# Optimization experiments

Measured on AMD Instinct MI355X. Metric: run time of the kernel, lower is better.

Reference implementation:

```python
import jax, jax.numpy as jnp
import numpy as np

NT, NRV, NR = 100000, 200000, 300000  # tile / road_vertex / road node counts
E = 400000                             # edges per edge type
B, H, P, A = 64, 128, 64, 512          # graphs, hidden, player_state_dim, action_dim


def _gat(h_src, h_dst, src, dst, W, a_s, a_d, b, n_dst):
    # PyG GATConv, heads=1, shared lin for src/dst, no self loops (bipartite)
    hs = h_src @ W                      # [Ns, H]
    hd = h_dst @ W                      # [Nd, H]
    e = jax.nn.leaky_relu((hs @ a_s)[src] + (hd @ a_d)[dst], 0.2)  # [E]
    m = jax.ops.segment_max(e, dst, num_segments=n_dst)
    w = jnp.exp(e - m[dst])
    denom = jax.ops.segment_sum(w, dst, num_segments=n_dst)
    alpha = w / jnp.maximum(denom[dst], 1e-16)                      # segment softmax
    out = jax.ops.segment_sum(alpha[:, None] * hs[src], dst, num_segments=n_dst)
    return out + b


def _mean_pool(x, batch, nb):
    s = jax.ops.segment_sum(x, batch, num_segments=nb)
    c = jax.ops.segment_sum(jnp.ones((x.shape[0],), x.dtype), batch, num_segments=nb)
    return s / jnp.maximum(c, 1.0)[:, None]


def setup_inputs():
    ks = iter(jax.random.split(jax.random.key(0), 64))
    f32 = jnp.float32

    def lin(i, o):
        return (jax.random.normal(next(ks), (i, o), f32) / np.float32(np.sqrt(i)))

    d = {}
    d['x_tile'] = jax.random.normal(next(ks), (NT, 8), f32)
    d['x_rv'] = jax.random.normal(next(ks), (NRV, 13), f32)
    d['x_road'] = jax.random.normal(next(ks), (NR, 4), f32)
    d['x_player'] = jax.random.normal(next(ks), (B, P), f32)
    # node encoders
    d['enc_t_W'] = lin(8, H);  d['enc_t_b'] = jnp.zeros((H,), f32)
    d['enc_rv_W'] = lin(13, H); d['enc_rv_b'] = jnp.zeros((H,), f32)
    d['enc_r_W'] = lin(4, H);  d['enc_r_b'] = jnp.zeros((H,), f32)
    # six GAT convs
    for name in ['rv2t', 't2rv', 'r2rv', 'rv2r', 't2r', 'r2t']:
        d[name + '_W'] = lin(H, H)
        d[name + '_as'] = jax.random.normal(next(ks), (H,), f32) * 0.1
        d[name + '_ad'] = jax.random.normal(next(ks), (H,), f32) * 0.1
        d[name + '_b'] = jnp.zeros((H,), f32)
    # player MLP + output head (input: 3H pooled + H player)
    d['fc1_W'] = lin(P, H); d['fc1_b'] = jnp.zeros((H,), f32)
    d['fc2_W'] = lin(H, H); d['fc2_b'] = jnp.zeros((H,), f32)
    d['out_W'] = lin(4 * H, A); d['out_b'] = jnp.zeros((A,), f32)
    # edges (src bounded by source-type count, dst by dest-type count)
    ri = lambda n, hi: jax.random.randint(n, (E,), 0, hi, jnp.int32)
    d['e_rv2t_src'] = ri(next(ks), NRV); d['e_rv2t_dst'] = ri(next(ks), NT)
    d['e_t2rv_src'] = ri(next(ks), NT);  d['e_t2rv_dst'] = ri(next(ks), NRV)
    d['e_r2rv_src'] = ri(next(ks), NR);  d['e_r2rv_dst'] = ri(next(ks), NRV)
    d['e_rv2r_src'] = ri(next(ks), NRV); d['e_rv2r_dst'] = ri(next(ks), NR)
    d['e_t2r_src'] = ri(next(ks), NT);   d['e_t2r_dst'] = ri(next(ks), NR)
    d['e_r2t_src'] = ri(next(ks), NR);   d['e_r2t_dst'] = ri(next(ks), NT)
    # batch assignment per node type
    d['batch_tile'] = jnp.sort(jax.random.randint(next(ks), (NT,), 0, B, jnp.int32))
    d['batch_rv'] = jnp.sort(jax.random.randint(next(ks), (NRV,), 0, B, jnp.int32))
    d['batch_road'] = jnp.sort(jax.random.randint(next(ks), (NR,), 0, B, jnp.int32))
    return d


def reference(x_tile, x_rv, x_road, x_player,
              enc_t_W, enc_t_b, enc_rv_W, enc_rv_b, enc_r_W, enc_r_b,
              rv2t_W, rv2t_as, rv2t_ad, rv2t_b,
              t2rv_W, t2rv_as, t2rv_ad, t2rv_b,
              r2rv_W, r2rv_as, r2rv_ad, r2rv_b,
              rv2r_W, rv2r_as, rv2r_ad, rv2r_b,
              t2r_W, t2r_as, t2r_ad, t2r_b,
              r2t_W, r2t_as, r2t_ad, r2t_b,
              fc1_W, fc1_b, fc2_W, fc2_b, out_W, out_b,
              e_rv2t_src, e_rv2t_dst, e_t2rv_src, e_t2rv_dst,
              e_r2rv_src, e_r2rv_dst, e_rv2r_src, e_rv2r_dst,
              e_t2r_src, e_t2r_dst, e_r2t_src, e_r2t_dst,
              batch_tile, batch_rv, batch_road):
    # node encoders
    h_t = x_tile @ enc_t_W + enc_t_b
    h_rv = x_rv @ enc_rv_W + enc_rv_b
    h_r = x_road @ enc_r_W + enc_r_b
    # hetero GAT, aggr='sum' over edge types per destination node type
    o_t = (_gat(h_rv, h_t, e_rv2t_src, e_rv2t_dst, rv2t_W, rv2t_as, rv2t_ad, rv2t_b, NT)
           + _gat(h_r, h_t, e_r2t_src, e_r2t_dst, r2t_W, r2t_as, r2t_ad, r2t_b, NT))
    o_rv = (_gat(h_t, h_rv, e_t2rv_src, e_t2rv_dst, t2rv_W, t2rv_as, t2rv_ad, t2rv_b, NRV)
            + _gat(h_r, h_rv, e_r2rv_src, e_r2rv_dst, r2rv_W, r2rv_as, r2rv_ad, r2rv_b, NRV))
    o_r = (_gat(h_rv, h_r, e_rv2r_src, e_rv2r_dst, rv2r_W, rv2r_as, rv2r_ad, rv2r_b, NR)
           + _gat(h_t, h_r, e_t2r_src, e_t2r_dst, t2r_W, t2r_as, t2r_ad, t2r_b, NR))
    # global mean pool per node type, concat -> [B, 3H]
    x_all = jnp.concatenate([_mean_pool(o_t, batch_tile, B),
                             _mean_pool(o_rv, batch_rv, B),
                             _mean_pool(o_r, batch_road, B)], axis=1)
    # player branch
    p = jax.nn.relu(x_player @ fc1_W + fc1_b)
    p = jax.nn.relu(p @ fc2_W + fc2_b)
    x = jnp.concatenate([x_all, p], axis=1)  # [B, 4H]
    return x @ out_W + out_b                 # [B, A]
```

## Files before the change

kernel.cpp:

```cpp
#include <hip/hip_runtime.h>


constexpr int kNT = 100000, kNRV = 200000, kNR = 300000, kE = 400000;
constexpr int kSLOT = 1088;
constexpr int kPSZ  = 6 * kSLOT;
constexpr int kNBE  = 342;
constexpr int kNTH  = kNBE * 256;
constexpr int kEPT  = 5;

constexpr long long OFF_C    = 0;
constexpr long long OFF_VS   = 13056;
constexpr long long OFF_VD   = 13176;
constexpr long long OFF_P    = 13296;
constexpr long long OFF_XCAT = 19824;
constexpr long long OFF_SRV  = 52592;
constexpr long long OFF_ST   = 3252592;
constexpr long long OFF_SR   = 4052592;
constexpr long long OFF_LDD  = 5252592;
constexpr long long OFF_P8   = 7652592;

__constant__ const int kDRB[6]   = {0, 100000, 300000, 500000, 800000, 1100000};
__constant__ const int kDLEN[6]  = {100000, 200000, 200000, 300000, 300000, 100000};
__constant__ const int kLSOFF[6] = {7, 4, 2, 8, 5, 3};
__constant__ const int kRSZ[6]   = {16, 8, 4, 16, 8, 4};

__device__ __forceinline__ int lowb(const int* a, int n, int v) {
  int lo = 0, hi = n;
  while (lo < hi) { int mid = (lo + hi) >> 1; if (a[mid] < v) lo = mid + 1; else hi = mid; }
  return lo;
}

static __device__ __forceinline__ unsigned p2h(float a, float b) {
  _Float16 ha = (_Float16)a, hb = (_Float16)b;
  unsigned short ua = __builtin_bit_cast(unsigned short, ha);
  unsigned short ub = __builtin_bit_cast(unsigned short, hb);
  return (unsigned)ua | ((unsigned)ub << 16);
}

static __device__ __forceinline__ float emb(float ld, int b) {
  return __uint_as_float((__float_as_uint(ld) & ~63u) | (unsigned)b);
}

__global__ __launch_bounds__(256) void precompute_kernel(
    const float* encW_t, const float* encb_t,
    const float* encW_rv, const float* encb_rv,
    const float* encW_r, const float* encb_r,
    const float* W0, const float* as0, const float* ad0,
    const float* W1, const float* as1, const float* ad1,
    const float* W2, const float* as2, const float* ad2,
    const float* W3, const float* as3, const float* ad3,
    const float* W4, const float* as4, const float* ad4,
    const float* W5, const float* as5, const float* ad5,
    float* Cws, float* vsw, float* vdw, float* P8)
{
  const float* encW[3] = {encW_t, encW_rv, encW_r};
  const float* encb[3] = {encb_t, encb_rv, encb_r};
  const int    Ks[3]   = {8, 13, 4};
  const float* Wv[6]  = {W0, W1, W2, W3, W4, W5};
  const float* asv[6] = {as0, as1, as2, as3, as4, as5};
  const float* adv[6] = {ad0, ad1, ad2, ad3, ad4, ad5};
  const int srcT[6] = {1, 0, 2, 1, 0, 2};
  const int dstT[6] = {0, 1, 1, 2, 2, 0};

  __shared__ float Cl[2176];
  __shared__ float wv[128];

  int et = blockIdx.x;
  int tid = threadIdx.x;
  int st = srcT[et], dt = dstT[et];
  const float* eW = encW[st];
  const float* eB = encb[st];
  int K = Ks[st];
  const float* W = Wv[et];
  const float* a_s = asv[et];
  const float* a_d = adv[et];
  float* Cslot = Cws + et * 2176;

  for (int c = 0; c < 8; ++c)
    for (int i = tid; i < kSLOT; i += 256)
      P8[c * kPSZ + et * kSLOT + i] = 0.f;

  for (int idx = tid; idx < (K + 1) * 128; idx += 256) {
    int r = idx >> 7, j = idx & 127;
    const float* row = (r < K) ? (eW + r * 128) : eB;
    float acc = 0.f;
    for (int m = 0; m < 128; ++m) acc += row[m] * W[m * 128 + j];
    int o = (r < K) ? (r * 128 + j) : (2048 + j);
    Cl[o] = acc;
    Cslot[o] = acc;
  }
  if (tid < 128) {
    float acc = 0.f;
    for (int j = 0; j < 128; ++j) acc += W[tid * 128 + j] * a_d[j];
    wv[tid] = acc;
  }
  __syncthreads();
  if (tid <= K) {
    const float* row = (tid < K) ? (Cl + tid * 128) : (Cl + 2048);
    float acc = 0.f;
    for (int j = 0; j < 128; ++j) acc += row[j] * a_s[j];
    vsw[et * 20 + (tid < K ? tid : 16)] = acc;
  }
  int KD = Ks[dt];
  if (tid >= 32 && tid <= 32 + KD) {
    int k = tid - 32;
    const float* row = (k < KD) ? (encW[dt] + k * 128) : encb[dt];
    float acc = 0.f;
    for (int m = 0; m < 128; ++m) acc += row[m] * wv[m];
    vdw[et * 20 + (k < KD ? k : 16)] = acc;
  }
}

__global__ __launch_bounds__(256) void prep_kernel(
    const float* __restrict__ x_t, const float* __restrict__ x_rv,
    const float* __restrict__ x_r,
    const int* __restrict__ bt, const int* __restrict__ brv,
    const int* __restrict__ br,
    const float* __restrict__ vsw, const float* __restrict__ vdw,
    uint4* __restrict__ SRVq, uint4* __restrict__ STq, uint4* __restrict__ SRq,
    float* __restrict__ LDDf)
{
  int n = blockIdx.x * 256 + threadIdx.x;
  if (n >= kNT + kNRV + kNR) return;
  if (n < kNT) {
    const float* xr = x_t + n * 8;
    int b = bt[n];
    const float* vsA = vsw + 1 * 20, *vsB = vsw + 4 * 20;
    const float* vdA = vdw + 0 * 20, *vdB = vdw + 5 * 20;
    float x[8]; float a0 = 0, a1 = 0, a2 = 0, a3 = 0;
#pragma unroll
    for (int k = 0; k < 8; ++k) {
      x[k] = xr[k];
      a0 += x[k] * vsA[k]; a1 += x[k] * vsB[k];
      a2 += x[k] * vdA[k]; a3 += x[k] * vdB[k];
    }
    float ls1 = a0 + vsA[16], ls4 = a1 + vsB[16];
    float ld0 = a2 + vdA[16], ld5 = a3 + vdB[16];
    STq[(long long)n * 2] =
        make_uint4(p2h(x[0], x[1]), p2h(x[2], x[3]), p2h(x[4], x[5]), p2h(x[6], x[7]));
    STq[(long long)n * 2 + 1] =
        make_uint4(__float_as_uint(ls1), __float_as_uint(ls4), 0, 0);
    LDDf[(long long)n * 2] = emb(ld0, b);
    LDDf[(long long)n * 2 + 1] = 0.f;
    LDDf[(long long)(1100000 + n) * 2] = emb(ld5, b);
    LDDf[(long long)(1100000 + n) * 2 + 1] = 0.f;
  } else if (n < kNT + kNRV) {
    int m = n - kNT;
    const float* xr = x_rv + m * 13;
    int b = brv[m];
    const float* vsA = vsw + 0 * 20, *vsB = vsw + 3 * 20;
    const float* vdA = vdw + 1 * 20, *vdB = vdw + 2 * 20;
    float x[13]; float a0 = 0, a1 = 0, a2 = 0, a3 = 0;
#pragma unroll
    for (int k = 0; k < 13; ++k) {
      x[k] = xr[k];
      a0 += x[k] * vsA[k]; a1 += x[k] * vsB[k];
      a2 += x[k] * vdA[k]; a3 += x[k] * vdB[k];
    }
    float ls0 = a0 + vsA[16], ls3 = a1 + vsB[16];
    float ld1 = a2 + vdA[16], ld2 = a3 + vdB[16];
    SRVq[(long long)m * 4] =
        make_uint4(p2h(x[0], x[1]), p2h(x[2], x[3]), p2h(x[4], x[5]), p2h(x[6], x[7]));
    SRVq[(long long)m * 4 + 1] =
        make_uint4(p2h(x[8], x[9]), p2h(x[10], x[11]), p2h(x[12], 0.f),
                   __float_as_uint(ls0));
    SRVq[(long long)m * 4 + 2] = make_uint4(__float_as_uint(ls3), 0, 0, 0);
    LDDf[(long long)(100000 + m) * 2] = emb(ld1, b);
    LDDf[(long long)(100000 + m) * 2 + 1] = 0.f;
    LDDf[(long long)(300000 + m) * 2] = emb(ld2, b);
    LDDf[(long long)(300000 + m) * 2 + 1] = 0.f;
  } else {
    int m = n - kNT - kNRV;
    const float* xr = x_r + m * 4;
    int b = br[m];
    const float* vsA = vsw + 2 * 20, *vsB = vsw + 5 * 20;
    const float* vdA = vdw + 3 * 20, *vdB = vdw + 4 * 20;
    float x[4]; float a0 = 0, a1 = 0, a2 = 0, a3 = 0;
#pragma unroll
    for (int k = 0; k < 4; ++k) {
      x[k] = xr[k];
      a0 += x[k] * vsA[k]; a1 += x[k] * vsB[k];
      a2 += x[k] * vdA[k]; a3 += x[k] * vdB[k];
    }
    float ls2 = a0 + vsA[16], ls5 = a1 + vsB[16];
    float ld3 = a2 + vdA[16], ld4 = a3 + vdB[16];
    SRq[m] = make_uint4(p2h(x[0], x[1]), p2h(x[2], x[3]),
                        __float_as_uint(ls2), __float_as_uint(ls5));
    LDDf[(long long)(500000 + m) * 2] = emb(ld3, b);
    LDDf[(long long)(500000 + m) * 2 + 1] = 0.f;
    LDDf[(long long)(800000 + m) * 2] = emb(ld4, b);
    LDDf[(long long)(800000 + m) * 2 + 1] = 0.f;
  }
}

__device__ __forceinline__ void pickSD(
    int et,
    const int* s0, const int* s1, const int* s2,
    const int* s3, const int* s4, const int* s5,
    const int* d0, const int* d1, const int* d2,
    const int* d3, const int* d4, const int* d5,
    const int*& sp, const int*& dp)
{
  switch (et) {
    case 0: sp = s0; dp = d0; break;
    case 1: sp = s1; dp = d1; break;
    case 2: sp = s2; dp = d2; break;
    case 3: sp = s3; dp = d3; break;
    case 4: sp = s4; dp = d4; break;
    default: sp = s5; dp = d5; break;
  }
}

__global__ __launch_bounds__(256, 8) void edgeA_kernel(
    const int* s0, const int* s1, const int* s2,
    const int* s3, const int* s4, const int* s5,
    const int* d0, const int* d1, const int* d2,
    const int* d3, const int* d4, const int* d5,
    const unsigned* __restrict__ SRVu, const unsigned* __restrict__ STu,
    const unsigned* __restrict__ SRu, float* __restrict__ LDDf)
{
  int et = blockIdx.x / kNBE;
  int bIdx = blockIdx.x - et * kNBE;
  const int* sp; const int* dp;
  pickSD(et, s0, s1, s2, s3, s4, s5, d0, d1, d2, d3, d4, d5, sp, dp);
  const unsigned* su = (et == 1 || et == 4) ? STu : ((et == 2 || et == 5) ? SRu : SRVu);
  const int rsz = kRSZ[et];
  const int lso = kLSOFF[et];
  const int drb = kDRB[et];
  int base = bIdx * 256 + (int)threadIdx.x;

  int s[kEPT], d[kEPT]; bool ok[kEPT];
#pragma unroll
  for (int j = 0; j < kEPT; ++j) {
    int e = base + j * kNTH;
    ok[j] = e < kE;
    int ee = ok[j] ? e : 0;
    s[j] = sp[ee]; d[j] = dp[ee];
  }
  float ls[kEPT];
#pragma unroll
  for (int j = 0; j < kEPT; ++j)
    ls[j] = __uint_as_float(su[(long long)s[j] * rsz + lso]);
  float ld[kEPT];
#pragma unroll
  for (int j = 0; j < kEPT; ++j)
    ld[j] = LDDf[(long long)(drb + d[j]) * 2];
#pragma unroll
  for (int j = 0; j < kEPT; ++j) {
    float t = ls[j] + ld[j];
    t = t > 0.f ? t : 0.2f * t;
    float w = __expf(t);
    if (ok[j]) unsafeAtomicAdd(&LDDf[(long long)(drb + d[j]) * 2 + 1], w);
  }
}

template <int TYPE, int RSEL>
__device__ __forceinline__ void ebflow(
    int bIdx,
    const int* __restrict__ sp, const int* __restrict__ dp,
    const uint4* __restrict__ srq, const float2* __restrict__ LDD2,
    int drb, int dlen, float* lp)
{
  constexpr int K = (TYPE == 0) ? 8 : ((TYPE == 1) ? 13 : 4);
  const int tid = threadIdx.x;
  const int lane = tid & 63;
  int base = bIdx * 256 + tid;

  int s[kEPT], d[kEPT]; bool ok[kEPT];
#pragma unroll
  for (int j = 0; j < kEPT; ++j) {
    int e = base + j * kNTH;
    ok[j] = e < kE;
    int ee = ok[j] ? e : 0;
    s[j] = sp[ee]; d[j] = dp[ee];
  }
  uint4 q0[kEPT], q1[kEPT];
  float lsx[kEPT];
#pragma unroll
  for (int j = 0; j < kEPT; ++j) {
    if (TYPE == 0) {
      q0[j] = srq[(long long)s[j] * 2];
      lsx[j] = __uint_as_float(
          ((const unsigned*)srq)[(long long)s[j] * 8 + (RSEL ? 5 : 4)]);
    } else if (TYPE == 1) {
      q0[j] = srq[(long long)s[j] * 4];
      q1[j] = srq[(long long)s[j] * 4 + 1];
      lsx[j] = RSEL
          ? __uint_as_float(((const unsigned*)srq)[(long long)s[j] * 16 + 8])
          : __uint_as_float(q1[j].w);
    } else {
      q0[j] = srq[s[j]];
      lsx[j] = __uint_as_float(RSEL ? q0[j].w : q0[j].z);
    }
  }
  float2 f2[kEPT];
#pragma unroll
  for (int j = 0; j < kEPT; ++j) f2[j] = LDD2[drb + d[j]];

#pragma unroll
  for (int j = 0; j < kEPT; ++j) {
    if (!ok[j]) continue;
    int b = (int)(__float_as_uint(f2[j].x) & 63u);
    float t = lsx[j] + f2[j].x;
    t = t > 0.f ? t : 0.2f * t;
    float w = __expf(t);
    float alpha = w / fmaxf(f2[j].y, 1e-16f);
    float xv[K];
    if (TYPE == 0) {
      const _Float16* h = (const _Float16*)&q0[j];
#pragma unroll
      for (int k = 0; k < 8; ++k) xv[k] = (float)h[k];
    } else if (TYPE == 1) {
      const _Float16* h = (const _Float16*)&q0[j];
#pragma unroll
      for (int k = 0; k < 8; ++k) xv[k] = (float)h[k];
      const _Float16* h2 = (const _Float16*)&q1[j];
#pragma unroll
      for (int k = 0; k < 5; ++k) xv[8 + k] = (float)h2[k];
    } else {
      const _Float16* h = (const _Float16*)&q0[j];
#pragma unroll
      for (int k = 0; k < 4; ++k) xv[k] = (float)h[k];
    }
#pragma unroll
    for (int k = 0; k < K; ++k) atomicAdd(lp + k * 64 + b, alpha * xv[k]);
  }

  for (int base2 = bIdx * 256 + (tid & ~63); base2 < dlen; base2 += kNTH) {
    int j2 = base2 + lane;
    bool a2 = j2 < dlen;
    float2 r2 = a2 ? LDD2[drb + j2] : make_float2(0.f, 0.f);
    int b2 = a2 ? (int)(__float_as_uint(r2.x) & 63u) : (64 + lane);
    int v = (a2 && r2.y > 0.f) ? 1 : 0;
#pragma unroll
    for (int d2 = 1; d2 < 64; d2 <<= 1) {
      int ob = __shfl_up(b2, d2);
      int ov = __shfl_up(v, d2);
      if (lane >= d2 && ob == b2) v += ov;
    }
    int bn = __shfl_down(b2, 1);
    if (((lane == 63) || (bn != b2)) && v > 0) atomicAdd(lp + 1024 + b2, (float)v);
  }
}

__global__ __launch_bounds__(256, 4) void edgeB_kernel(
    const int* s0, const int* s1, const int* s2,
    const int* s3, const int* s4, const int* s5,
    const int* d0, const int* d1, const int* d2,
    const int* d3, const int* d4, const int* d5,
    const uint4* SRVq, const uint4* STq, const uint4* SRq,
    const float2* __restrict__ LDD2, float* __restrict__ P8)
{
  __shared__ float lp[kSLOT];
  for (int j = threadIdx.x; j < kSLOT; j += 256) lp[j] = 0.f;
  __syncthreads();
  int et = blockIdx.x / kNBE;
  int bIdx = blockIdx.x - et * kNBE;
  constexpr int KK[6] = {13, 8, 4, 13, 8, 4};
  switch (et) {
    case 0: ebflow<1, 0>(bIdx, s0, d0, SRVq, LDD2, 0,       100000, lp); break;
    case 1: ebflow<0, 0>(bIdx, s1, d1, STq,  LDD2, 100000,  200000, lp); break;
    case 2: ebflow<2, 0>(bIdx, s2, d2, SRq,  LDD2, 300000,  200000, lp); break;
    case 3: ebflow<1, 1>(bIdx, s3, d3, SRVq, LDD2, 500000,  300000, lp); break;
    case 4: ebflow<0, 1>(bIdx, s4, d4, STq,  LDD2, 800000,  300000, lp); break;
    default: ebflow<2, 1>(bIdx, s5, d5, SRq, LDD2, 1100000, 100000, lp); break;
  }
  __syncthreads();
  int K = KK[et];
  float* slab = P8 + (long long)(blockIdx.x & 7) * kPSZ + (long long)et * kSLOT;
  for (int i = threadIdx.x; i < kSLOT; i += 256) {
    if (i >= K * 64 && i < 1024) continue;
    float v = lp[i];
    if (v != 0.f) unsafeAtomicAdd(&slab[i], v);
  }
}

__global__ __launch_bounds__(256) void reduceP8_kernel(
    const float* __restrict__ P8, float* __restrict__ P)
{
  int j = blockIdx.x * 256 + threadIdx.x;
  if (j >= kPSZ) return;
  float s = 0.f;
#pragma unroll
  for (int c = 0; c < 8; ++c) s += P8[c * kPSZ + j];
  P[j] = s;
}

__global__ __launch_bounds__(128) void finalize_kernel(
    const int* __restrict__ bt, const int* __restrict__ brv, const int* __restrict__ br,
    const float* __restrict__ xp,
    const float* __restrict__ fc1W, const float* __restrict__ fc1b,
    const float* __restrict__ fc2W, const float* __restrict__ fc2b,
    const float* __restrict__ b_rv2t, const float* __restrict__ b_r2t,
    const float* __restrict__ b_t2rv, const float* __restrict__ b_r2rv,
    const float* __restrict__ b_rv2r, const float* __restrict__ b_t2r,
    const float* __restrict__ Cws, const float* __restrict__ P,
    float* __restrict__ xcat)
{
  int b = blockIdx.x, tid = threadIdx.x;
  __shared__ float xps[64];
  __shared__ float p1s[128];
  __shared__ int cnts[3];
  if (tid < 64) xps[tid] = xp[b * 64 + tid];
  if (tid < 3) {
    const int* ba = (tid == 0) ? bt : (tid == 1 ? brv : br);
    int N = (tid == 0) ? kNT : (tid == 1 ? kNRV : kNR);
    cnts[tid] = lowb(ba, N, b + 1) - lowb(ba, N, b);
  }
  __syncthreads();
  float a = fc1b[tid];
  for (int k = 0; k < 64; ++k) a += xps[k] * fc1W[k * 128 + tid];
  p1s[tid] = fmaxf(a, 0.f);
  __syncthreads();
  float a2 = fc2b[tid];
  for (int k = 0; k < 128; ++k) a2 += p1s[k] * fc2W[k * 128 + tid];
  xcat[b * 512 + 384 + tid] = fmaxf(a2, 0.f);
  const int etA[3] = {0, 1, 3}, etB[3] = {5, 2, 4};
  const int KAv[3] = {13, 8, 13}, KBv[3] = {4, 4, 8};
  for (int t3 = 0; t3 < 3; ++t3) {
    int eA = etA[t3], eB = etB[t3];
    const float* CA = Cws + eA * 2176;
    const float* CB = Cws + eB * 2176;
    const float* pA = P + eA * kSLOT;
    const float* pB = P + eB * kSLOT;
    float cA = pA[1024 + b];
    float cB = pB[1024 + b];
    float v = cA * CA[2048 + tid] + cB * CB[2048 + tid];
    for (int k = 0; k < KAv[t3]; ++k) v += pA[k * 64 + b] * CA[k * 128 + tid];
    for (int k = 0; k < KBv[t3]; ++k) v += pB[k * 64 + b] * CB[k * 128 + tid];
    float cnt = (float)max(cnts[t3], 1);
    const float* bb1 = (t3 == 0) ? b_rv2t : (t3 == 1 ? b_t2rv : b_rv2r);
    const float* bb2 = (t3 == 0) ? b_r2t  : (t3 == 1 ? b_r2rv : b_t2r);
    xcat[b * 512 + t3 * 128 + tid] = v / cnt + bb1[tid] + bb2[tid];
  }
}

__global__ __launch_bounds__(256) void out_kernel(
    const float* __restrict__ xcat, const float* __restrict__ outW,
    const float* __restrict__ outb, float* __restrict__ out)
{
  int g = blockIdx.x * 256 + threadIdx.x;
  int r = g >> 9, c = g & 511;
  const float* xr = xcat + r * 512;
  float acc = outb[c];
  for (int k = 0; k < 512; ++k) acc += xr[k] * outW[k * 512 + c];
  out[g] = acc;
}

extern "C" void kernel_launch(void* const* d_in, const int* in_sizes, int n_in,
                              void* d_out, int out_size, void* d_ws, size_t ws_size,
                              hipStream_t stream) {
  const float* x_tile   = (const float*)d_in[0];
  const float* x_rv     = (const float*)d_in[1];
  const float* x_road   = (const float*)d_in[2];
  const float* x_player = (const float*)d_in[3];
  const float* enc_t_W  = (const float*)d_in[4];
  const float* enc_t_b  = (const float*)d_in[5];
  const float* enc_rv_W = (const float*)d_in[6];
  const float* enc_rv_b = (const float*)d_in[7];
  const float* enc_r_W  = (const float*)d_in[8];
  const float* enc_r_b  = (const float*)d_in[9];
  const float* W[6]; const float* As[6]; const float* Ad[6]; const float* Bb[6];
  for (int et = 0; et < 6; ++et) {
    W[et]  = (const float*)d_in[10 + 4 * et];
    As[et] = (const float*)d_in[11 + 4 * et];
    Ad[et] = (const float*)d_in[12 + 4 * et];
    Bb[et] = (const float*)d_in[13 + 4 * et];
  }
  const float* fc1W = (const float*)d_in[34];
  const float* fc1b = (const float*)d_in[35];
  const float* fc2W = (const float*)d_in[36];
  const float* fc2b = (const float*)d_in[37];
  const float* outW = (const float*)d_in[38];
  const float* outb = (const float*)d_in[39];
  const int* esrc[6]; const int* edst[6];
  for (int et = 0; et < 6; ++et) {
    esrc[et] = (const int*)d_in[40 + 2 * et];
    edst[et] = (const int*)d_in[41 + 2 * et];
  }
  const int* batch_t  = (const int*)d_in[52];
  const int* batch_rv = (const int*)d_in[53];
  const int* batch_r  = (const int*)d_in[54];

  float* wsF = (float*)d_ws;
  float* Cws  = wsF + OFF_C;
  float* vsw  = wsF + OFF_VS;
  float* vdw  = wsF + OFF_VD;
  float* P    = wsF + OFF_P;
  float* xcat = wsF + OFF_XCAT;
  uint4* SRVq = (uint4*)(wsF + OFF_SRV);
  uint4* STq  = (uint4*)(wsF + OFF_ST);
  uint4* SRq  = (uint4*)(wsF + OFF_SR);
  float* LDDf = wsF + OFF_LDD;
  float2* LDD2 = (float2*)(wsF + OFF_LDD);
  float* P8   = wsF + OFF_P8;
  float* out  = (float*)d_out;

  precompute_kernel<<<6, 256, 0, stream>>>(
      enc_t_W, enc_t_b, enc_rv_W, enc_rv_b, enc_r_W, enc_r_b,
      W[0], As[0], Ad[0], W[1], As[1], Ad[1], W[2], As[2], Ad[2],
      W[3], As[3], Ad[3], W[4], As[4], Ad[4], W[5], As[5], Ad[5],
      Cws, vsw, vdw, P8);

  prep_kernel<<<(kNT + kNRV + kNR + 255) / 256, 256, 0, stream>>>(
      x_tile, x_rv, x_road, batch_t, batch_rv, batch_r, vsw, vdw,
      SRVq, STq, SRq, LDDf);

  edgeA_kernel<<<6 * kNBE, 256, 0, stream>>>(
      esrc[0], esrc[1], esrc[2], esrc[3], esrc[4], esrc[5],
      edst[0], edst[1], edst[2], edst[3], edst[4], edst[5],
      (const unsigned*)SRVq, (const unsigned*)STq, (const unsigned*)SRq, LDDf);

  edgeB_kernel<<<6 * kNBE, 256, 0, stream>>>(
      esrc[0], esrc[1], esrc[2], esrc[3], esrc[4], esrc[5],
      edst[0], edst[1], edst[2], edst[3], edst[4], edst[5],
      SRVq, STq, SRq, LDD2, P8);

  reduceP8_kernel<<<(kPSZ + 255) / 256, 256, 0, stream>>>(P8, P);

  finalize_kernel<<<64, 128, 0, stream>>>(
      batch_t, batch_rv, batch_r, x_player,
      fc1W, fc1b, fc2W, fc2b,
      Bb[0], Bb[5], Bb[1], Bb[2], Bb[3], Bb[4],
      Cws, P, xcat);

  out_kernel<<<128, 256, 0, stream>>>(xcat, outW, outb, out);

  (void)in_sizes; (void)n_in; (void)out_size; (void)ws_size;
}
```

Before: 527.0 us.

## Fuse P8 reduction, finalize and output GEMM into one tail kernel; compact source logits

The reduceP8, finalize and out kernels are merged into a single tail kernel with one block per graph. Each block recomputes the encoder-times-W projections in shared memory and sums the eight P8 partial copies itself, which cuts two launches and the xcat round trip. Precompute now only folds W with the attention vectors, and its P8 zeroing is spread across all six blocks. prep writes a compact float array of source logits, so edgeA gathers 4-byte values instead of reading them from strided packed rows. The cost is redundant per-block projection work (64 blocks doing the same 128x128 by K products) and low parallelism in the fused output GEMM.

```diff
diff --git a/kernel.cpp b/kernel.cpp
--- a/kernel.cpp
+++ b/kernel.cpp
@@ -8,21 +8,18 @@
 constexpr int kNTH  = kNBE * 256;
 constexpr int kEPT  = 5;
 
-constexpr long long OFF_C    = 0;
-constexpr long long OFF_VS   = 13056;
-constexpr long long OFF_VD   = 13176;
-constexpr long long OFF_P    = 13296;
-constexpr long long OFF_XCAT = 19824;
-constexpr long long OFF_SRV  = 52592;
-constexpr long long OFF_ST   = 3252592;
-constexpr long long OFF_SR   = 4052592;
-constexpr long long OFF_LDD  = 5252592;
-constexpr long long OFF_P8   = 7652592;
-
-__constant__ const int kDRB[6]   = {0, 100000, 300000, 500000, 800000, 1100000};
-__constant__ const int kDLEN[6]  = {100000, 200000, 200000, 300000, 300000, 100000};
-__constant__ const int kLSOFF[6] = {7, 4, 2, 8, 5, 3};
-__constant__ const int kRSZ[6]   = {16, 8, 4, 16, 8, 4};
+constexpr long long OFF_VS   = 0;
+constexpr long long OFF_VD   = 120;
+constexpr long long OFF_P8   = 256;
+constexpr long long OFF_LS6  = 52480;
+constexpr long long OFF_SRV  = 652480;
+constexpr long long OFF_ST   = 3852480;
+constexpr long long OFF_SR   = 4652480;
+constexpr long long OFF_LDD  = 5852480;
+
+__constant__ const int kDRB[6]  = {0, 100000, 300000, 500000, 800000, 1100000};
+__constant__ const int kDLEN[6] = {100000, 200000, 200000, 300000, 300000, 100000};
+__constant__ const int kLSB6[6] = {0, 400000, 0, 200000, 500000, 0};
 
 __device__ __forceinline__ int lowb(const int* a, int n, int v) {
   int lo = 0, hi = n;
@@ -51,7 +48,7 @@
     const float* W3, const float* as3, const float* ad3,
     const float* W4, const float* as4, const float* ad4,
     const float* W5, const float* as5, const float* ad5,
-    float* Cws, float* vsw, float* vdw, float* P8)
+    float* vsw, float* vdw, float* P8)
 {
   const float* encW[3] = {encW_t, encW_rv, encW_r};
   const float* encb[3] = {encb_t, encb_rv, encb_r};
@@ -62,43 +59,34 @@
   const int srcT[6] = {1, 0, 2, 1, 0, 2};
   const int dstT[6] = {0, 1, 1, 2, 2, 0};
 
-  __shared__ float Cl[2176];
-  __shared__ float wv[128];
+  __shared__ float ws[128], wd[128];
 
   int et = blockIdx.x;
   int tid = threadIdx.x;
   int st = srcT[et], dt = dstT[et];
-  const float* eW = encW[st];
-  const float* eB = encb[st];
-  int K = Ks[st];
   const float* W = Wv[et];
   const float* a_s = asv[et];
   const float* a_d = adv[et];
-  float* Cslot = Cws + et * 2176;
-
-  for (int c = 0; c < 8; ++c)
-    for (int i = tid; i < kSLOT; i += 256)
-      P8[c * kPSZ + et * kSLOT + i] = 0.f;
-
-  for (int idx = tid; idx < (K + 1) * 128; idx += 256) {
-    int r = idx >> 7, j = idx & 127;
-    const float* row = (r < K) ? (eW + r * 128) : eB;
+
+  for (int i = et * 256 + tid; i < 8 * kPSZ; i += 6 * 256) P8[i] = 0.f;
+
+  if (tid < 128) {
+    float accs = 0.f, accd = 0.f;
+    const float* row = W + tid * 128;
+    for (int j = 0; j < 128; ++j) {
+      float w = row[j];
+      accs += w * a_s[j];
+      accd += w * a_d[j];
+    }
+    ws[tid] = accs;
+    wd[tid] = accd;
+  }
+  __syncthreads();
+  int K = Ks[st];
+  if (tid <= K) {
+    const float* row = (tid < K) ? (encW[st] + tid * 128) : encb[st];
     float acc = 0.f;
-    for (int m = 0; m < 128; ++m) acc += row[m] * W[m * 128 + j];
-    int o = (r < K) ? (r * 128 + j) : (2048 + j);
-    Cl[o] = acc;
-    Cslot[o] = acc;
-  }
-  if (tid < 128) {
-    float acc = 0.f;
-    for (int j = 0; j < 128; ++j) acc += W[tid * 128 + j] * a_d[j];
-    wv[tid] = acc;
-  }
-  __syncthreads();
-  if (tid <= K) {
-    const float* row = (tid < K) ? (Cl + tid * 128) : (Cl + 2048);
-    float acc = 0.f;
-    for (int j = 0; j < 128; ++j) acc += row[j] * a_s[j];
+    for (int m = 0; m < 128; ++m) acc += row[m] * ws[m];
     vsw[et * 20 + (tid < K ? tid : 16)] = acc;
   }
   int KD = Ks[dt];
@@ -106,7 +94,7 @@
     int k = tid - 32;
     const float* row = (k < KD) ? (encW[dt] + k * 128) : encb[dt];
     float acc = 0.f;
-    for (int m = 0; m < 128; ++m) acc += row[m] * wv[m];
+    for (int m = 0; m < 128; ++m) acc += row[m] * wd[m];
     vdw[et * 20 + (k < KD ? k : 16)] = acc;
   }
 }
@@ -118,7 +106,7 @@
     const int* __restrict__ br,
     const float* __restrict__ vsw, const float* __restrict__ vdw,
     uint4* __restrict__ SRVq, uint4* __restrict__ STq, uint4* __restrict__ SRq,
-    float* __restrict__ LDDf)
+    float* __restrict__ LS6, float* __restrict__ LDDf)
 {
   int n = blockIdx.x * 256 + threadIdx.x;
   if (n >= kNT + kNRV + kNR) return;
@@ -140,6 +128,8 @@
         make_uint4(p2h(x[0], x[1]), p2h(x[2], x[3]), p2h(x[4], x[5]), p2h(x[6], x[7]));
     STq[(long long)n * 2 + 1] =
         make_uint4(__float_as_uint(ls1), __float_as_uint(ls4), 0, 0);
+    LS6[400000 + n] = ls1;
+    LS6[500000 + n] = ls4;
     LDDf[(long long)n * 2] = emb(ld0, b);
     LDDf[(long long)n * 2 + 1] = 0.f;
     LDDf[(long long)(1100000 + n) * 2] = emb(ld5, b);
@@ -165,6 +155,8 @@
         make_uint4(p2h(x[8], x[9]), p2h(x[10], x[11]), p2h(x[12], 0.f),
                    __float_as_uint(ls0));
     SRVq[(long long)m * 4 + 2] = make_uint4(__float_as_uint(ls3), 0, 0, 0);
+    LS6[m] = ls0;
+    LS6[200000 + m] = ls3;
     LDDf[(long long)(100000 + m) * 2] = emb(ld1, b);
     LDDf[(long long)(100000 + m) * 2 + 1] = 0.f;
     LDDf[(long long)(300000 + m) * 2] = emb(ld2, b);
@@ -216,16 +208,13 @@
     const int* s3, const int* s4, const int* s5,
     const int* d0, const int* d1, const int* d2,
     const int* d3, const int* d4, const int* d5,
-    const unsigned* __restrict__ SRVu, const unsigned* __restrict__ STu,
-    const unsigned* __restrict__ SRu, float* __restrict__ LDDf)
+    const unsigned* __restrict__ SRu, const float* __restrict__ LS6,
+    float* __restrict__ LDDf)
 {
   int et = blockIdx.x / kNBE;
   int bIdx = blockIdx.x - et * kNBE;
   const int* sp; const int* dp;
   pickSD(et, s0, s1, s2, s3, s4, s5, d0, d1, d2, d3, d4, d5, sp, dp);
-  const unsigned* su = (et == 1 || et == 4) ? STu : ((et == 2 || et == 5) ? SRu : SRVu);
-  const int rsz = kRSZ[et];
-  const int lso = kLSOFF[et];
   const int drb = kDRB[et];
   int base = bIdx * 256 + (int)threadIdx.x;
 
@@ -238,9 +227,16 @@
     s[j] = sp[ee]; d[j] = dp[ee];
   }
   float ls[kEPT];
-#pragma unroll
-  for (int j = 0; j < kEPT; ++j)
-    ls[j] = __uint_as_float(su[(long long)s[j] * rsz + lso]);
+  if (et == 2 || et == 5) {
+    const int lso = (et == 2) ? 2 : 3;
+#pragma unroll
+    for (int j = 0; j < kEPT; ++j)
+      ls[j] = __uint_as_float(SRu[(long long)s[j] * 4 + lso]);
+  } else {
+    const float* L = LS6 + kLSB6[et];
+#pragma unroll
+    for (int j = 0; j < kEPT; ++j) ls[j] = L[s[j]];
+  }
   float ld[kEPT];
 #pragma unroll
   for (int j = 0; j < kEPT; ++j)
@@ -375,76 +371,114 @@
   }
 }
 
-__global__ __launch_bounds__(256) void reduceP8_kernel(
-    const float* __restrict__ P8, float* __restrict__ P)
-{
-  int j = blockIdx.x * 256 + threadIdx.x;
-  if (j >= kPSZ) return;
-  float s = 0.f;
-#pragma unroll
-  for (int c = 0; c < 8; ++c) s += P8[c * kPSZ + j];
-  P[j] = s;
-}
-
-__global__ __launch_bounds__(128) void finalize_kernel(
+template <int K>
+__device__ __forceinline__ void colC(
+    const float* __restrict__ W, const float* __restrict__ eW,
+    const float* __restrict__ eb, int tid, float* __restrict__ outCol)
+{
+  float acc[K + 1];
+#pragma unroll
+  for (int k = 0; k <= K; ++k) acc[k] = 0.f;
+  for (int m = 0; m < 128; ++m) {
+    float w = W[m * 128 + tid];
+#pragma unroll
+    for (int k = 0; k < K; ++k) acc[k] += eW[k * 128 + m] * w;
+    acc[K] += eb[m] * w;
+  }
+#pragma unroll
+  for (int k = 0; k <= K; ++k) outCol[k * 128 + tid] = acc[k];
+}
+
+__global__ __launch_bounds__(128) void tail_kernel(
     const int* __restrict__ bt, const int* __restrict__ brv, const int* __restrict__ br,
     const float* __restrict__ xp,
     const float* __restrict__ fc1W, const float* __restrict__ fc1b,
     const float* __restrict__ fc2W, const float* __restrict__ fc2b,
+    const float* __restrict__ outW, const float* __restrict__ outb,
+    const float* W0, const float* W1, const float* W2,
+    const float* W3, const float* W4, const float* W5,
+    const float* encW_t, const float* encb_t,
+    const float* encW_rv, const float* encb_rv,
+    const float* encW_r, const float* encb_r,
     const float* __restrict__ b_rv2t, const float* __restrict__ b_r2t,
     const float* __restrict__ b_t2rv, const float* __restrict__ b_r2rv,
     const float* __restrict__ b_rv2r, const float* __restrict__ b_t2r,
-    const float* __restrict__ Cws, const float* __restrict__ P,
-    float* __restrict__ xcat)
+    const float* __restrict__ P8, float* __restrict__ out)
 {
   int b = blockIdx.x, tid = threadIdx.x;
+  __shared__ float C[56 * 128];
+  __shared__ float xrow[512];
+  __shared__ float p1s[128];
   __shared__ float xps[64];
-  __shared__ float p1s[128];
+  __shared__ float psA[15], psB[15];
   __shared__ int cnts[3];
+
   if (tid < 64) xps[tid] = xp[b * 64 + tid];
-  if (tid < 3) {
-    const int* ba = (tid == 0) ? bt : (tid == 1 ? brv : br);
-    int N = (tid == 0) ? kNT : (tid == 1 ? kNRV : kNR);
-    cnts[tid] = lowb(ba, N, b + 1) - lowb(ba, N, b);
-  }
+  if (tid >= 64 && tid < 67) {
+    int t = tid - 64;
+    const int* ba = (t == 0) ? bt : (t == 1 ? brv : br);
+    int N = (t == 0) ? kNT : (t == 1 ? kNRV : kNR);
+    cnts[t] = lowb(ba, N, b + 1) - lowb(ba, N, b);
+  }
+
+  colC<13>(W0, encW_rv, encb_rv, tid, C + 0 * 128);
+  colC<8>(W1, encW_t, encb_t, tid, C + 14 * 128);
+  colC<4>(W2, encW_r, encb_r, tid, C + 23 * 128);
+  colC<13>(W3, encW_rv, encb_rv, tid, C + 28 * 128);
+  colC<8>(W4, encW_t, encb_t, tid, C + 42 * 128);
+  colC<4>(W5, encW_r, encb_r, tid, C + 51 * 128);
   __syncthreads();
+
   float a = fc1b[tid];
   for (int k = 0; k < 64; ++k) a += xps[k] * fc1W[k * 128 + tid];
   p1s[tid] = fmaxf(a, 0.f);
   __syncthreads();
   float a2 = fc2b[tid];
   for (int k = 0; k < 128; ++k) a2 += p1s[k] * fc2W[k * 128 + tid];
-  xcat[b * 512 + 384 + tid] = fmaxf(a2, 0.f);
+  xrow[384 + tid] = fmaxf(a2, 0.f);
+
   const int etA[3] = {0, 1, 3}, etB[3] = {5, 2, 4};
+  const int bA[3] = {0, 14, 28}, bB[3] = {51, 23, 42};
   const int KAv[3] = {13, 8, 13}, KBv[3] = {4, 4, 8};
   for (int t3 = 0; t3 < 3; ++t3) {
+    __syncthreads();
     int eA = etA[t3], eB = etB[t3];
-    const float* CA = Cws + eA * 2176;
-    const float* CB = Cws + eB * 2176;
-    const float* pA = P + eA * kSLOT;
-    const float* pB = P + eB * kSLOT;
-    float cA = pA[1024 + b];
-    float cB = pB[1024 + b];
-    float v = cA * CA[2048 + tid] + cB * CB[2048 + tid];
-    for (int k = 0; k < KAv[t3]; ++k) v += pA[k * 64 + b] * CA[k * 128 + tid];
-    for (int k = 0; k < KBv[t3]; ++k) v += pB[k * 64 + b] * CB[k * 128 + tid];
+    if (tid < 15) {
+      int idx = (tid < 14) ? (tid * 64 + b) : (1024 + b);
+      float sum = 0.f;
+#pragma unroll
+      for (int c = 0; c < 8; ++c) sum += P8[c * kPSZ + eA * kSLOT + idx];
+      psA[tid] = sum;
+    } else if (tid < 30) {
+      int t = tid - 15;
+      int idx = (t < 14) ? (t * 64 + b) : (1024 + b);
+      float sum = 0.f;
+#pragma unroll
+      for (int c = 0; c < 8; ++c) sum += P8[c * kPSZ + eB * kSLOT + idx];
+      psB[t] = sum;
+    }
+    __syncthreads();
+    int KA = KAv[t3], KB = KBv[t3];
+    const float* CA = C + bA[t3] * 128;
+    const float* CB = C + bB[t3] * 128;
+    float v = psA[14] * CA[KA * 128 + tid] + psB[14] * CB[KB * 128 + tid];
+    for (int k = 0; k < KA; ++k) v += psA[k] * CA[k * 128 + tid];
+    for (int k = 0; k < KB; ++k) v += psB[k] * CB[k * 128 + tid];
     float cnt = (float)max(cnts[t3], 1);
     const float* bb1 = (t3 == 0) ? b_rv2t : (t3 == 1 ? b_t2rv : b_rv2r);
     const float* bb2 = (t3 == 0) ? b_r2t  : (t3 == 1 ? b_r2rv : b_t2r);
-    xcat[b * 512 + t3 * 128 + tid] = v / cnt + bb1[tid] + bb2[tid];
-  }
-}
-
-__global__ __launch_bounds__(256) void out_kernel(
-    const float* __restrict__ xcat, const float* __restrict__ outW,
-    const float* __restrict__ outb, float* __restrict__ out)
-{
-  int g = blockIdx.x * 256 + threadIdx.x;
-  int r = g >> 9, c = g & 511;
-  const float* xr = xcat + r * 512;
-  float acc = outb[c];
-  for (int k = 0; k < 512; ++k) acc += xr[k] * outW[k * 512 + c];
-  out[g] = acc;
+    xrow[t3 * 128 + tid] = v / cnt + bb1[tid] + bb2[tid];
+  }
+  __syncthreads();
+
+#pragma unroll
+  for (int q = 0; q < 4; ++q) {
+    int c = q * 128 + tid;
+    float acc = outb[c];
+#pragma unroll 8
+    for (int k = 0; k < 512; ++k) acc += xrow[k] * outW[k * 512 + c];
+    out[b * 512 + c] = acc;
+  }
 }
 
 extern "C" void kernel_launch(void* const* d_in, const int* in_sizes, int n_in,
@@ -483,48 +517,44 @@
   const int* batch_r  = (const int*)d_in[54];
 
   float* wsF = (float*)d_ws;
-  float* Cws  = wsF + OFF_C;
   float* vsw  = wsF + OFF_VS;
   float* vdw  = wsF + OFF_VD;
-  float* P    = wsF + OFF_P;
-  float* xcat = wsF + OFF_XCAT;
+  float* P8   = wsF + OFF_P8;
+  float* LS6  = wsF + OFF_LS6;
   uint4* SRVq = (uint4*)(wsF + OFF_SRV);
   uint4* STq  = (uint4*)(wsF + OFF_ST);
   uint4* SRq  = (uint4*)(wsF + OFF_SR);
   float* LDDf = wsF + OFF_LDD;
   float2* LDD2 = (float2*)(wsF + OFF_LDD);
-  float* P8   = wsF + OFF_P8;
   float* out  = (float*)d_out;
 
   precompute_kernel<<<6, 256, 0, stream>>>(
       enc_t_W, enc_t_b, enc_rv_W, enc_rv_b, enc_r_W, enc_r_b,
       W[0], As[0], Ad[0], W[1], As[1], Ad[1], W[2], As[2], Ad[2],
       W[3], As[3], Ad[3], W[4], As[4], Ad[4], W[5], As[5], Ad[5],
-      Cws, vsw, vdw, P8);
+      vsw, vdw, P8);
 
   prep_kernel<<<(kNT + kNRV + kNR + 255) / 256, 256, 0, stream>>>(
       x_tile, x_rv, x_road, batch_t, batch_rv, batch_r, vsw, vdw,
-      SRVq, STq, SRq, LDDf);
+      SRVq, STq, SRq, LS6, LDDf);
 
   edgeA_kernel<<<6 * kNBE, 256, 0, stream>>>(
       esrc[0], esrc[1], esrc[2], esrc[3], esrc[4], esrc[5],
       edst[0], edst[1], edst[2], edst[3], edst[4], edst[5],
-      (const unsigned*)SRVq, (const unsigned*)STq, (const unsigned*)SRq, LDDf);
+      (const unsigned*)SRq, LS6, LDDf);
 
   edgeB_kernel<<<6 * kNBE, 256, 0, stream>>>(
       esrc[0], esrc[1], esrc[2], esrc[3], esrc[4], esrc[5],
       edst[0], edst[1], edst[2], edst[3], edst[4], edst[5],
       SRVq, STq, SRq, LDD2, P8);
 
-  reduceP8_kernel<<<(kPSZ + 255) / 256, 256, 0, stream>>>(P8, P);
-
-  finalize_kernel<<<64, 128, 0, stream>>>(
+  tail_kernel<<<64, 128, 0, stream>>>(
       batch_t, batch_rv, batch_r, x_player,
-      fc1W, fc1b, fc2W, fc2b,
+      fc1W, fc1b, fc2W, fc2b, outW, outb,
+      W[0], W[1], W[2], W[3], W[4], W[5],
+      enc_t_W, enc_t_b, enc_rv_W, enc_rv_b, enc_r_W, enc_r_b,
       Bb[0], Bb[5], Bb[1], Bb[2], Bb[3], Bb[4],
-      Cws, P, xcat);
-
-  out_kernel<<<128, 256, 0, stream>>>(xcat, outW, outb, out);
+      P8, out);
 
   (void)in_sizes; (void)n_in; (void)out_size; (void)ws_size;
 }
```

Measured after the change: 638.0 us. 1.21x slower.
